# Optimization experiments

Measured on AMD Instinct MI355X. Metric: run time of the kernel, lower is better.

Reference implementation:

```python
import jax, jax.numpy as jnp
import numpy as np


def setup_inputs() -> dict:
    key = jax.random.key(0)
    k1, k2 = jax.random.split(key)
    B, L = 8192, 4096
    v = jax.random.normal(k1, (B, L), dtype=jnp.float32)
    z = jax.random.normal(k2, (B, L), dtype=jnp.float32)
    return {"v": v, "z": z}


def reference(v, z):
    # Householder reflection: z_new = z - 2 * v (v . z) / ||v||^2
    # Mathematically identical to the original bmm(v v^T, z) formulation,
    # but contracts the rank-1 outer product analytically (no BxLxL tensor).
    vz = jnp.sum(v * z, axis=1, keepdims=True)        # [B, 1] = v . z per row
    norm_sq = jnp.sum(v * v, axis=1, keepdims=True)    # [B, 1] = ||v||^2
    return z - 2.0 * v * (vz / norm_sq)
```

## Files before the change

kernel.cpp:

```cpp
#include <hip/hip_runtime.h>
#include <hip/hip_bf16.h>


#define L_DIM 4096
#define BLOCK 256
#define VEC (L_DIM / 4)
#define PER_THREAD (VEC / BLOCK)

__global__ __launch_bounds__(BLOCK) void householder_kernel(
    const float* __restrict__ v,
    const float* __restrict__ z,
    float* __restrict__ out)
{
    __shared__ float4 sv[VEC];
    __shared__ float4 sz[VEC];
    __shared__ float s_red[2][4];
    __shared__ float s_scale;

    const int row = blockIdx.x;
    const size_t base = (size_t)row * L_DIM;
    const float4* v4 = (const float4*)(v + base);
    const float4* z4 = (const float4*)(z + base);
    float4* o4 = (float4*)(out + base);

    float vz = 0.0f, vv = 0.0f;

    #pragma unroll
    for (int k = 0; k < PER_THREAD; ++k) {
        const int i = threadIdx.x + k * BLOCK;
        float4 a = v4[i];
        float4 b = z4[i];
        sv[i] = a;
        sz[i] = b;
        vz = fmaf(a.x, b.x, vz); vz = fmaf(a.y, b.y, vz);
        vz = fmaf(a.z, b.z, vz); vz = fmaf(a.w, b.w, vz);
        vv = fmaf(a.x, a.x, vv); vv = fmaf(a.y, a.y, vv);
        vv = fmaf(a.z, a.z, vv); vv = fmaf(a.w, a.w, vv);
    }

    #pragma unroll
    for (int off = 32; off > 0; off >>= 1) {
        vz += __shfl_down(vz, off, 64);
        vv += __shfl_down(vv, off, 64);
    }

    const int wave = threadIdx.x >> 6;
    const int lane = threadIdx.x & 63;
    if (lane == 0) {
        s_red[0][wave] = vz;
        s_red[1][wave] = vv;
    }
    __syncthreads();

    if (threadIdx.x == 0) {
        float tvz = s_red[0][0] + s_red[0][1] + s_red[0][2] + s_red[0][3];
        float tvv = s_red[1][0] + s_red[1][1] + s_red[1][2] + s_red[1][3];
        s_scale = -2.0f * tvz / tvv;
    }
    __syncthreads();

    const float s = s_scale;

    #pragma unroll
    for (int k = 0; k < PER_THREAD; ++k) {
        const int i = threadIdx.x + k * BLOCK;
        float4 a = sv[i];
        float4 b = sz[i];
        float4 r;
        r.x = fmaf(s, a.x, b.x);
        r.y = fmaf(s, a.y, b.y);
        r.z = fmaf(s, a.z, b.z);
        r.w = fmaf(s, a.w, b.w);
        o4[i] = r;
    }
}

extern "C" void kernel_launch(void* const* d_in, const int* in_sizes, int n_in,
                              void* d_out, int out_size, void* d_ws, size_t ws_size,
                              hipStream_t stream) {
    const float* v = (const float*)d_in[0];
    const float* z = (const float*)d_in[1];
    float* out = (float*)d_out;
    const int B = in_sizes[0] / L_DIM;
    householder_kernel<<<B, BLOCK, 0, stream>>>(v, z, out);
}
```

Baseline: 304.9 us.

## Keep row data in registers, widen block, and use nontemporal output stores

Drops the 32 KB per-block LDS staging of v and z and holds each thread's elements in registers instead. The block grows to 512 threads with 2 float4 per thread. Every thread now sums the per-wave partials itself, which removes the second barrier. Output is written with nontemporal stores so it does not pollute the cache. The aim is higher occupancy, since LDS no longer limits blocks per CU, and fewer LDS round trips in this bandwidth-bound kernel. In exchange it uses more registers and does redundant reduction work in every thread.

Measured after the change: 313.5 us. 1.03x slower.

```diff
diff --git a/kernel.cpp b/kernel.cpp
--- a/kernel.cpp
+++ b/kernel.cpp
@@ -1,41 +1,44 @@
 #include <hip/hip_runtime.h>
-#include <hip/hip_bf16.h>
 
 
 #define L_DIM 4096
-#define BLOCK 256
+#define BLOCK 512
 #define VEC (L_DIM / 4)
 #define PER_THREAD (VEC / BLOCK)
+#define NWAVES (BLOCK / 64)
+
+typedef float f4 __attribute__((ext_vector_type(4)));
 
 __global__ __launch_bounds__(BLOCK) void householder_kernel(
     const float* __restrict__ v,
     const float* __restrict__ z,
-    float* __restrict__ out)
+    float* __restrict__ out,
+    int B)
 {
-    __shared__ float4 sv[VEC];
-    __shared__ float4 sz[VEC];
-    __shared__ float s_red[2][4];
-    __shared__ float s_scale;
+    __shared__ float s_red[2][NWAVES];
 
     const int row = blockIdx.x;
+    if (row >= B) return;
     const size_t base = (size_t)row * L_DIM;
-    const float4* v4 = (const float4*)(v + base);
-    const float4* z4 = (const float4*)(z + base);
-    float4* o4 = (float4*)(out + base);
+    const f4* v4 = (const f4*)(v + base);
+    const f4* z4 = (const f4*)(z + base);
+    f4* o4 = (f4*)(out + base);
 
-    float vz = 0.0f, vv = 0.0f;
-
+    f4 a[PER_THREAD], b[PER_THREAD];
     #pragma unroll
     for (int k = 0; k < PER_THREAD; ++k) {
         const int i = threadIdx.x + k * BLOCK;
-        float4 a = v4[i];
-        float4 b = z4[i];
-        sv[i] = a;
-        sz[i] = b;
-        vz = fmaf(a.x, b.x, vz); vz = fmaf(a.y, b.y, vz);
-        vz = fmaf(a.z, b.z, vz); vz = fmaf(a.w, b.w, vz);
-        vv = fmaf(a.x, a.x, vv); vv = fmaf(a.y, a.y, vv);
-        vv = fmaf(a.z, a.z, vv); vv = fmaf(a.w, a.w, vv);
+        a[k] = v4[i];
+        b[k] = z4[i];
+    }
+
+    float vz = 0.0f, vv = 0.0f;
+    #pragma unroll
+    for (int k = 0; k < PER_THREAD; ++k) {
+        vz = fmaf(a[k].x, b[k].x, vz); vz = fmaf(a[k].y, b[k].y, vz);
+        vz = fmaf(a[k].z, b[k].z, vz); vz = fmaf(a[k].w, b[k].w, vz);
+        vv = fmaf(a[k].x, a[k].x, vv); vv = fmaf(a[k].y, a[k].y, vv);
+        vv = fmaf(a[k].z, a[k].z, vv); vv = fmaf(a[k].w, a[k].w, vv);
     }
 
     #pragma unroll
@@ -45,33 +48,29 @@
     }
 
     const int wave = threadIdx.x >> 6;
-    const int lane = threadIdx.x & 63;
-    if (lane == 0) {
+    if ((threadIdx.x & 63) == 0) {
         s_red[0][wave] = vz;
         s_red[1][wave] = vv;
     }
     __syncthreads();
 
-    if (threadIdx.x == 0) {
-        float tvz = s_red[0][0] + s_red[0][1] + s_red[0][2] + s_red[0][3];
-        float tvv = s_red[1][0] + s_red[1][1] + s_red[1][2] + s_red[1][3];
-        s_scale = -2.0f * tvz / tvv;
+    float tvz = 0.0f, tvv = 0.0f;
+    #pragma unroll
+    for (int w = 0; w < NWAVES; ++w) {
+        tvz += s_red[0][w];
+        tvv += s_red[1][w];
     }
-    __syncthreads();
-
-    const float s = s_scale;
+    const float s = -2.0f * tvz / tvv;
 
     #pragma unroll
     for (int k = 0; k < PER_THREAD; ++k) {
         const int i = threadIdx.x + k * BLOCK;
-        float4 a = sv[i];
-        float4 b = sz[i];
-        float4 r;
-        r.x = fmaf(s, a.x, b.x);
-        r.y = fmaf(s, a.y, b.y);
-        r.z = fmaf(s, a.z, b.z);
-        r.w = fmaf(s, a.w, b.w);
-        o4[i] = r;
+        f4 r;
+        r.x = fmaf(s, a[k].x, b[k].x);
+        r.y = fmaf(s, a[k].y, b[k].y);
+        r.z = fmaf(s, a[k].z, b[k].z);
+        r.w = fmaf(s, a[k].w, b[k].w);
+        __builtin_nontemporal_store(r, &o4[i]);
     }
 }
 
@@ -82,5 +81,5 @@
     const float* z = (const float*)d_in[1];
     float* out = (float*)d_out;
     const int B = in_sizes[0] / L_DIM;
-    householder_kernel<<<B, BLOCK, 0, stream>>>(v, z, out);
+    householder_kernel<<<B, BLOCK, 0, stream>>>(v, z, out, B);
 }
```
